# Optimization experiments

Hardware: AMD Instinct MI355X
Metric: run time of the kernel (lower is better)

## Reference

```python
import jax, jax.numpy as jnp
import numpy as np

H = 8        # num_heads
L = 2        # num_layers
F = 9        # num_fields
D = 128      # n_field_info
DH = D       # per-head depth = (D*H)//H
NB = 50      # n_base
EXCL = (0, 1, 2)  # fields excluded in FinalMerge (SelfAttention_Ex0, n_fields-3 inputs)
EPS = 1e-5


def _ln(x, g, b):
    m = jnp.mean(x, -1, keepdims=True)
    v = jnp.mean((x - m) ** 2, -1, keepdims=True)
    return (x - m) / jnp.sqrt(v + EPS) * g + b


def _forward(Y, Gin, posW1, posB1, posW2, posB2, posW3, posB3,
             Wq, bq, Wk, bk, Wv, bv, Wo, bo, lnG, lnB, fnG, fnB, poolW,
             uQW, uQB, uKW, uKB, uVW, uVB, mQW, mQB, mKW, mKB, mVW, mVB):
    B, S, _ = Y.shape
    pooled = []
    for f in range(F):  # per-field towers are structurally distinct (separate params)
        gy = jnp.concatenate([Y, Gin[:, :, f:f + 1]], axis=-1)        # [B,S,NB+1]
        h = jnp.tanh(gy @ posW1[f].T + posB1[f])
        h = jnp.tanh(h @ posW2[f].T + posB2[f])
        x = jax.nn.sigmoid(h @ posW3[f].T + posB3[f])                  # [B,S,D]
        for l in range(L):
            q = (x @ Wq[l, f].T + bq[l, f]).reshape(B, S, H, DH).transpose(0, 2, 1, 3)
            k = (x @ Wk[l, f].T + bk[l, f]).reshape(B, S, H, DH).transpose(0, 2, 1, 3)
            v = (x @ Wv[l, f].T + bv[l, f]).reshape(B, S, H, DH).transpose(0, 2, 1, 3)
            att = jax.nn.softmax(jnp.einsum('bhsd,bhtd->bhst', q, k) / jnp.sqrt(jnp.float32(DH)), axis=-1)
            wv = jnp.einsum('bhst,bhtd->bhsd', att, v).transpose(0, 2, 1, 3).reshape(B, S, H * DH)
            out = wv @ Wo[l, f].T + bo[l, f]
            x = _ln(x + out, lnG[l, f], lnB[l, f])   # residual + per-field LayerNorm
        x = _ln(x, fnG, fnB)                         # final_norm
        sc = jax.nn.softmax(x @ poolW[f][:, None], axis=1)             # GlobalAttentionPooling, [B,S,1]
        pooled.append(jnp.sum(x * sc, axis=1))                         # [B,D]
    U = jnp.stack(pooled, axis=-1)                                     # [B,D,F]

    unified = []
    for f in range(F):  # SelfAttention per target field
        Q = U @ uQW[f].T + uQB[f]                                      # [B,D,D]
        K = U @ uKW[f].T + uKB[f]
        V = U @ uVW[f].T + uVB[f]
        A = jax.nn.softmax(jnp.einsum('bik,bjk->bij', Q, K) / jnp.sqrt(jnp.float32(F)), axis=-1)
        o = jnp.einsum('bij,bjk->bik', A, V).mean(axis=-1)             # [B,D]
        o = o + (U[:, :, f] if f > 0 else U.mean(axis=-1))
        unified.append(o)
    Uu = jnp.stack(unified, axis=-1)                                   # [B,D,F]

    inc = [i for i in range(F) if i not in EXCL]
    Us = U[:, :, jnp.array(inc)]                                       # [B,D,F-3]
    Q = Us @ mQW.T + mQB
    K = Us @ mKW.T + mKB
    V = Us @ mVW.T + mVB
    A = jax.nn.softmax(jnp.einsum('bik,bjk->bij', Q, K) / jnp.sqrt(jnp.float32(F)), axis=-1)
    g = jnp.einsum('bij,bjk->bik', A, V).mean(axis=-1) + Us.mean(axis=-1)  # [B,D]
    return jnp.concatenate([Uu, g[:, :, None]], axis=-1)               # [B,D,F+1]


def setup_inputs() -> dict:
    key = jax.random.key(0)
    ks = iter(jax.random.split(key, 64))
    nrm = lambda shape, s=1.0: jax.random.normal(next(ks), shape, dtype=jnp.float32) * s
    B, S = 8, 512
    d = {}
    d['Y'] = nrm((B, S, NB))
    d['Gin'] = nrm((B, S, F))
    d['posW1'] = nrm((F, 50, NB + 1), 0.14); d['posB1'] = jnp.zeros((F, 50))
    d['posW2'] = nrm((F, 50, 50), 0.14);     d['posB2'] = jnp.zeros((F, 50))
    d['posW3'] = nrm((F, D, 50), 0.14);      d['posB3'] = jnp.zeros((F, D))
    d['Wq'] = nrm((L, F, H * DH, D), 0.09);  d['bq'] = jnp.zeros((L, F, H * DH))
    d['Wk'] = nrm((L, F, H * DH, D), 0.09);  d['bk'] = jnp.zeros((L, F, H * DH))
    d['Wv'] = nrm((L, F, H * DH, D), 0.09);  d['bv'] = jnp.zeros((L, F, H * DH))
    d['Wo'] = nrm((L, F, D, H * DH), 0.03);  d['bo'] = jnp.zeros((L, F, D))
    d['lnG'] = jnp.ones((L, F, D)); d['lnB'] = jnp.zeros((L, F, D))
    d['fnG'] = jnp.ones((D,));      d['fnB'] = jnp.zeros((D,))
    d['poolW'] = nrm((F, D))
    d['uQW'] = nrm((F, D, F), 0.33); d['uQB'] = jnp.zeros((F, D))
    d['uKW'] = nrm((F, D, F), 0.33); d['uKB'] = jnp.zeros((F, D))
    d['uVW'] = nrm((F, D, F), 0.33); d['uVB'] = jnp.zeros((F, D))
    d['mQW'] = nrm((D, F - 3), 0.4); d['mQB'] = jnp.zeros((D,))
    d['mKW'] = nrm((D, F - 3), 0.4); d['mKB'] = jnp.zeros((D,))
    d['mVW'] = nrm((D, F - 3), 0.4); d['mVB'] = jnp.zeros((D,))
    return d


def reference(Y, Gin, posW1, posB1, posW2, posB2, posW3, posB3,
              Wq, bq, Wk, bk, Wv, bv, Wo, bo, lnG, lnB, fnG, fnB, poolW,
              uQW, uQB, uKW, uKB, uVW, uVB, mQW, mQB, mKW, mKB, mVW, mVB):
    return _forward(Y, Gin, posW1, posB1, posW2, posB2, posW3, posB3,
                    Wq, bq, Wk, bk, Wv, bv, Wo, bo, lnG, lnB, fnG, fnB, poolW,
                    uQW, uQB, uKW, uKB, uVW, uVB, mQW, mQB, mKW, mKB, mVW, mVB)
```

## Files before the change

### kernel.cpp

```cpp
#include <hip/hip_runtime.h>
#include <hip/hip_bf16.h>

#define F_  9
#define B_  8
#define S_  512
#define H_  8
#define DH_ 128
#define D_  128
#define NB_ 50
#define BS_ 4096
#define PERBUF 4194304UL
#define WELEMS 2359296UL

typedef short bf16x8 __attribute__((ext_vector_type(8)));
typedef float f32x4  __attribute__((ext_vector_type(4)));
typedef unsigned int u32x4 __attribute__((ext_vector_type(4)));

static __device__ __forceinline__ unsigned short f2b(float f) {
    unsigned int u = __float_as_uint(f);
    unsigned int r = (u + 0x7FFFu + ((u >> 16) & 1u)) >> 16;
    return (unsigned short)r;
}
static __device__ __forceinline__ float b2f(unsigned short u) {
    return __uint_as_float(((unsigned int)u) << 16);
}
static __device__ __forceinline__ unsigned int cvtpk(float lo, float hi) {
    unsigned int r;
    asm("v_cvt_pk_bf16_f32 %0, %1, %2" : "=v"(r) : "v"(lo), "v"(hi));
    return r;
}

__global__ __launch_bounds__(256) void cvt4_kernel(
    const float* __restrict__ s0, const float* __restrict__ s1,
    const float* __restrict__ s2, const float* __restrict__ s3,
    unsigned short* __restrict__ d0, unsigned short* __restrict__ d1,
    unsigned short* __restrict__ d2, unsigned short* __restrict__ d3, int n)
{
    const float* s; unsigned short* d;
    switch (blockIdx.y) {
        case 0: s = s0; d = d0; break;
        case 1: s = s1; d = d1; break;
        case 2: s = s2; d = d2; break;
        default: s = s3; d = d3; break;
    }
    int i = (blockIdx.x * 256 + threadIdx.x) * 8;
    if (i + 8 <= n) {
        float4 a = *(const float4*)&s[i];
        float4 b = *(const float4*)&s[i + 4];
        ushort4 o0 = { f2b(a.x), f2b(a.y), f2b(a.z), f2b(a.w) };
        ushort4 o1 = { f2b(b.x), f2b(b.y), f2b(b.z), f2b(b.w) };
        *(ushort4*)&d[i]     = o0;
        *(ushort4*)&d[i + 4] = o1;
    }
}

__global__ __launch_bounds__(256) void posnet_kernel(
    const float* __restrict__ Y, const float* __restrict__ Gin,
    const float* __restrict__ W1g, const float* __restrict__ B1,
    const float* __restrict__ W2g, const float* __restrict__ B2,
    const float* __restrict__ W3g, const float* __restrict__ B3,
    float* __restrict__ xA, unsigned short* __restrict__ xAb)
{
    __shared__ float gys[4][8][52];
    __shared__ float hs[4][8][52];

    int f = blockIdx.y;
    int t = threadIdx.x, w = t >> 6, j = t & 63;
    int rowbase = blockIdx.x * 32 + w * 8;

#pragma unroll
    for (int rr = 0; rr < 8; ++rr) {
        int row = rowbase + rr;
        if (j < 50)       gys[w][rr][j]  = Y[(size_t)row*50 + j];
        else if (j == 50) gys[w][rr][50] = Gin[(size_t)row*F_ + f];
    }

    int jj = (j < 50) ? j : 0;

    {
        const float* wp = W1g + f*2550 + jj*51;
        float wreg[51];
#pragma unroll
        for (int kk = 0; kk < 51; ++kk) wreg[kk] = wp[kk];
        float bb = B1[f*50 + jj];
        float acc[8];
#pragma unroll
        for (int rr = 0; rr < 8; ++rr) acc[rr] = bb;
#pragma unroll
        for (int k4 = 0; k4 < 48; k4 += 4) {
#pragma unroll
            for (int rr = 0; rr < 8; ++rr) {
                float4 gv = *(const float4*)&gys[w][rr][k4];
                acc[rr] += wreg[k4]*gv.x + wreg[k4+1]*gv.y + wreg[k4+2]*gv.z + wreg[k4+3]*gv.w;
            }
        }
#pragma unroll
        for (int kk = 48; kk < 51; ++kk)
#pragma unroll
            for (int rr = 0; rr < 8; ++rr) acc[rr] += wreg[kk]*gys[w][rr][kk];
        if (j < 50) {
#pragma unroll
            for (int rr = 0; rr < 8; ++rr) hs[w][rr][j] = tanhf(acc[rr]);
        }
    }

    {
        const float* wp = W2g + f*2500 + jj*50;
        float wreg[50];
#pragma unroll
        for (int kk = 0; kk < 50; ++kk) wreg[kk] = wp[kk];
        float bb = B2[f*50 + jj];
        float acc[8];
#pragma unroll
        for (int rr = 0; rr < 8; ++rr) acc[rr] = bb;
#pragma unroll
        for (int k4 = 0; k4 < 48; k4 += 4) {
#pragma unroll
            for (int rr = 0; rr < 8; ++rr) {
                float4 gv = *(const float4*)&hs[w][rr][k4];
                acc[rr] += wreg[k4]*gv.x + wreg[k4+1]*gv.y + wreg[k4+2]*gv.z + wreg[k4+3]*gv.w;
            }
        }
#pragma unroll
        for (int kk = 48; kk < 50; ++kk)
#pragma unroll
            for (int rr = 0; rr < 8; ++rr) acc[rr] += wreg[kk]*hs[w][rr][kk];
        if (j < 50) {
#pragma unroll
            for (int rr = 0; rr < 8; ++rr) gys[w][rr][j] = tanhf(acc[rr]);
        }
    }

#pragma unroll 1
    for (int ppass = 0; ppass < 2; ++ppass) {
        const float* wp = W3g + f*6400 + (ppass*64 + j)*50;
        float wreg[50];
#pragma unroll
        for (int kk = 0; kk < 50; ++kk) wreg[kk] = wp[kk];
        float bb = B3[f*128 + ppass*64 + j];
        float acc[8];
#pragma unroll
        for (int rr = 0; rr < 8; ++rr) acc[rr] = bb;
#pragma unroll
        for (int k4 = 0; k4 < 48; k4 += 4) {
#pragma unroll
            for (int rr = 0; rr < 8; ++rr) {
                float4 gv = *(const float4*)&gys[w][rr][k4];
                acc[rr] += wreg[k4]*gv.x + wreg[k4+1]*gv.y + wreg[k4+2]*gv.z + wreg[k4+3]*gv.w;
            }
        }
#pragma unroll
        for (int kk = 48; kk < 50; ++kk)
#pragma unroll
            for (int rr = 0; rr < 8; ++rr) acc[rr] += wreg[kk]*gys[w][rr][kk];
#pragma unroll
        for (int rr = 0; rr < 8; ++rr) {
            float x = 1.f / (1.f + expf(-acc[rr]));
            size_t roff = ((size_t)f*BS_ + rowbase + rr)*128 + ppass*64 + j;
            xA[roff]  = x;
            xAb[roff] = f2b(x);
        }
    }
}

__global__ __launch_bounds__(256) void qkv_mfma_kernel(
    const unsigned short* __restrict__ xb,
    const unsigned short* __restrict__ Wqb, const unsigned short* __restrict__ Wkb,
    const unsigned short* __restrict__ Wvb,
    const float* __restrict__ bq, const float* __restrict__ bk, const float* __restrict__ bv,
    unsigned short* __restrict__ qo, unsigned short* __restrict__ ko,
    unsigned int* __restrict__ vto, int l, int f0)
{
    int z = blockIdx.z;
    int fl = z / 3, which = z - fl*3;
    int f = f0 + fl;
    const unsigned short* W; const float* bias;
    if (which == 0)      { W = Wqb; bias = bq; }
    else if (which == 1) { W = Wkb; bias = bk; }
    else                 { W = Wvb; bias = bv; }
    W    += (size_t)(l*F_ + f) * 1024 * 128;
    bias += (size_t)(l*F_ + f) * 1024;

    int m0 = blockIdx.x * 128;
    int n0 = blockIdx.y * 128;
    int t = threadIdx.x, w = t >> 6, ln = t & 63, g = ln >> 4, c = ln & 15;
    int wr = w >> 1, wc = w & 1;

    const unsigned short* Ab = xb + ((size_t)f*BS_ + m0 + wr*64)*128;
    const unsigned short* Bb = W + (size_t)(n0 + wc*64)*128;

    f32x4 acc[4][4];
#pragma unroll
    for (int mi = 0; mi < 4; ++mi)
#pragma unroll
        for (int ni = 0; ni < 4; ++ni) acc[mi][ni] = (f32x4){0.f,0.f,0.f,0.f};

#pragma unroll
    for (int kt = 0; kt < 4; ++kt) {
        bf16x8 af[4], bfr[4];
#pragma unroll
        for (int mi = 0; mi < 4; ++mi)
            af[mi] = *(const bf16x8*)&Ab[(size_t)(mi*16 + c)*128 + kt*32 + g*8];
#pragma unroll
        for (int ni = 0; ni < 4; ++ni)
            bfr[ni] = *(const bf16x8*)&Bb[(size_t)(ni*16 + c)*128 + kt*32 + g*8];
#pragma unroll
        for (int mi = 0; mi < 4; ++mi)
#pragma unroll
            for (int ni = 0; ni < 4; ++ni)
                acc[mi][ni] = __builtin_amdgcn_mfma_f32_16x16x32_bf16(af[mi], bfr[ni], acc[mi][ni], 0, 0, 0);
    }

    int h = n0 >> 7;
    float bs_[4];
#pragma unroll
    for (int ni = 0; ni < 4; ++ni) bs_[ni] = bias[n0 + wc*64 + ni*16 + c];

    if (which < 2) {
        float qscale = (which == 0) ? 0.08838834764831845f : 1.0f;
        unsigned short* out = (which == 0 ? qo : ko) + (size_t)fl * PERBUF;
#pragma unroll
        for (int mi = 0; mi < 4; ++mi) {
#pragma unroll
            for (int r = 0; r < 4; ++r) {
                int m = m0 + wr*64 + mi*16 + 4*g + r;
                int b = m >> 9, s = m & 511;
                unsigned short* orow = out + (((size_t)(b*H_ + h))*S_ + s)*128;
#pragma unroll
                for (int ni = 0; ni < 4; ++ni)
                    orow[wc*64 + ni*16 + c] = f2b((acc[mi][ni][r] + bs_[ni]) * qscale);
            }
        }
    } else {
        unsigned int* vtf = vto + (size_t)fl * (PERBUF/2);
#pragma unroll
        for (int mi = 0; mi < 4; ++mi) {
            int mbase = m0 + wr*64 + mi*16 + 4*g;
            int b = mbase >> 9, sh = (mbase & 511) >> 1;
            unsigned int* vtp = vtf + ((size_t)(b*H_ + h))*32768;
#pragma unroll
            for (int ni = 0; ni < 4; ++ni) {
                int d = wc*64 + ni*16 + c;
                float bb_ = bs_[ni];
                unsigned int p01 = (unsigned int)f2b(acc[mi][ni][0] + bb_)
                                 | ((unsigned int)f2b(acc[mi][ni][1] + bb_) << 16);
                unsigned int p23 = (unsigned int)f2b(acc[mi][ni][2] + bb_)
                                 | ((unsigned int)f2b(acc[mi][ni][3] + bb_) << 16);
                vtp[(size_t)d*256 + sh]     = p01;
                vtp[(size_t)d*256 + sh + 1] = p23;
            }
        }
    }
}

__global__ __launch_bounds__(256) void attn_mfma_kernel(
    const unsigned short* __restrict__ q, const unsigned short* __restrict__ k,
    const unsigned int* __restrict__ vt, unsigned short* __restrict__ wv)
{
    int t = threadIdx.x;
    int w = t >> 6, ln = t & 63, g = ln >> 4, c = ln & 15;
    int bid = blockIdx.x;
    int group = bid >> 5, within = bid & 31;
    int i = within >> 3, hl = within & 7;
    int hIdx = group*8 + hl;
    int fl = hIdx >> 6, by = hIdx & 63;
    int q0 = i*128 + w*32;

    const unsigned short* qh = q + ((size_t)(fl*64 + by))*S_*128;
    const unsigned short* kh = k + ((size_t)(fl*64 + by))*S_*128;
    const unsigned int*  vth = vt + ((size_t)(fl*64 + by))*32768;
    int b = by >> 3, h = by & 7;
    unsigned short* wvh = wv + ((size_t)(fl*B_ + b))*S_*1024 + h*128;

    __shared__ alignas(16) unsigned short Ks[2][32][136];
    __shared__ alignas(16) unsigned int   Vs[2][128][20];

    int krow = t >> 4, kseg = t & 15;
    int vrow = t >> 2, vseg = t & 3;

    bf16x8 qf[2][4];
#pragma unroll
    for (int gq = 0; gq < 2; ++gq)
#pragma unroll
        for (int d0 = 0; d0 < 4; ++d0)
            qf[gq][d0] = *(const bf16x8*)&qh[(size_t)(q0 + gq*16 + c)*128 + d0*32 + g*8];

    f32x4 acc[2][8];
#pragma unroll
    for (int gq = 0; gq < 2; ++gq)
#pragma unroll
        for (int i2 = 0; i2 < 8; ++i2) acc[gq][i2] = (f32x4){0.f, 0.f, 0.f, 0.f};
    float mrow[2] = {-1e30f, -1e30f};
    float lrow[2] = {0.f, 0.f};

    int srcA = ((g & 1) << 5) + c;
    int srcB = srcA + 16;
    bool glow = (g < 2);

    uint4 kr0, kr1, vr0, vr1;
    {
        kr0 = *(const uint4*)&kh[(size_t)krow*128 + kseg*8];
        kr1 = *(const uint4*)&kh[(size_t)(krow + 16)*128 + kseg*8];
        vr0 = *(const uint4*)&vth[(size_t)vrow*256 + vseg*4];
        vr1 = *(const uint4*)&vth[(size_t)(vrow + 64)*256 + vseg*4];
        *(uint4*)&Ks[0][krow][kseg*8]      = kr0;
        *(uint4*)&Ks[0][krow + 16][kseg*8] = kr1;
        *(uint4*)&Vs[0][vrow][vseg*4]      = vr0;
        *(uint4*)&Vs[0][vrow + 64][vseg*4] = vr1;
    }
    __syncthreads();

    int cur = 0;
    for (int kt = 0; kt < 16; ++kt) {
        if (kt < 15) {
            const unsigned short* ks = kh + (size_t)(kt + 1)*32*128;
            const unsigned int*  vsp = vth + (kt + 1)*16;
            kr0 = *(const uint4*)&ks[(size_t)krow*128 + kseg*8];
            kr1 = *(const uint4*)&ks[(size_t)(krow + 16)*128 + kseg*8];
            vr0 = *(const uint4*)&vsp[(size_t)vrow*256 + vseg*4];
            vr1 = *(const uint4*)&vsp[(size_t)(vrow + 64)*256 + vseg*4];
        }

        f32x4 s[2][2];
        s[0][0] = (f32x4){0.f,0.f,0.f,0.f}; s[0][1] = (f32x4){0.f,0.f,0.f,0.f};
        s[1][0] = (f32x4){0.f,0.f,0.f,0.f}; s[1][1] = (f32x4){0.f,0.f,0.f,0.f};
        __builtin_amdgcn_s_setprio(1);
#pragma unroll
        for (int d0 = 0; d0 < 4; ++d0) {
            bf16x8 k0 = *(const bf16x8*)&Ks[cur][c][g*8 + d0*32];
            bf16x8 k1 = *(const bf16x8*)&Ks[cur][16 + c][g*8 + d0*32];
#pragma unroll
            for (int gq = 0; gq < 2; ++gq) {
                s[gq][0] = __builtin_amdgcn_mfma_f32_16x16x32_bf16(k0, qf[gq][d0], s[gq][0], 0, 0, 0);
                s[gq][1] = __builtin_amdgcn_mfma_f32_16x16x32_bf16(k1, qf[gq][d0], s[gq][1], 0, 0, 0);
            }
        }
        __builtin_amdgcn_s_setprio(0);

        float corr[2];
        bf16x8 pa[2];
        bool need = false;
#pragma unroll
        for (int gq = 0; gq < 2; ++gq) {
            float t0 = fmaxf(fmaxf(fmaxf(s[gq][0][0], s[gq][0][1]), fmaxf(s[gq][0][2], s[gq][0][3])),
                             fmaxf(fmaxf(s[gq][1][0], s[gq][1][1]), fmaxf(s[gq][1][2], s[gq][1][3])));
            t0 = fmaxf(t0, __shfl_xor(t0, 16));
            t0 = fmaxf(t0, __shfl_xor(t0, 32));
            float mo = mrow[gq];
            float mn = (t0 > mo + 8.f) ? t0 : mo;
            float co = __expf(mo - mn);
            corr[gq] = co;
            mrow[gq] = mn;
            float p00 = __expf(s[gq][0][0] - mn), p01 = __expf(s[gq][0][1] - mn);
            float p02 = __expf(s[gq][0][2] - mn), p03 = __expf(s[gq][0][3] - mn);
            float p10 = __expf(s[gq][1][0] - mn), p11 = __expf(s[gq][1][1] - mn);
            float p12 = __expf(s[gq][1][2] - mn), p13 = __expf(s[gq][1][3] - mn);
            float ps = ((p00 + p01) + (p02 + p03)) + ((p10 + p11) + (p12 + p13));
            ps += __shfl_xor(ps, 16);
            ps += __shfl_xor(ps, 32);
            lrow[gq] = lrow[gq]*co + ps;
            need = need || (co != 1.0f);

            unsigned int pk0 = cvtpk(p00, p01), pk1 = cvtpk(p02, p03);
            unsigned int pk2 = cvtpk(p10, p11), pk3 = cvtpk(p12, p13);
            unsigned int a0 = __shfl(pk0, srcA), a1 = __shfl(pk1, srcA);
            unsigned int b0 = __shfl(pk0, srcB), b1 = __shfl(pk1, srcB);
            unsigned int c0 = __shfl(pk2, srcA), c1 = __shfl(pk3, srcA);
            unsigned int d0_ = __shfl(pk2, srcB), d1_ = __shfl(pk3, srcB);
            u32x4 pu;
            pu[0] = glow ? a0 : c0;
            pu[1] = glow ? a1 : c1;
            pu[2] = glow ? b0 : d0_;
            pu[3] = glow ? b1 : d1_;
            pa[gq] = __builtin_bit_cast(bf16x8, pu);
        }

        if (__any(need)) {
#pragma unroll
            for (int gq = 0; gq < 2; ++gq) {
                float cr0 = __shfl(corr[gq], 4*g + 0);
                float cr1 = __shfl(corr[gq], 4*g + 1);
                float cr2 = __shfl(corr[gq], 4*g + 2);
                float cr3 = __shfl(corr[gq], 4*g + 3);
#pragma unroll
                for (int i2 = 0; i2 < 8; ++i2) {
                    f32x4 a = acc[gq][i2];
                    a[0] *= cr0; a[1] *= cr1; a[2] *= cr2; a[3] *= cr3;
                    acc[gq][i2] = a;
                }
            }
        }

        __builtin_amdgcn_s_setprio(1);
#pragma unroll
        for (int i2 = 0; i2 < 8; ++i2) {
            bf16x8 vf = *(const bf16x8*)&Vs[cur][i2*16 + c][g*4];
            acc[0][i2] = __builtin_amdgcn_mfma_f32_16x16x32_bf16(pa[0], vf, acc[0][i2], 0, 0, 0);
            acc[1][i2] = __builtin_amdgcn_mfma_f32_16x16x32_bf16(pa[1], vf, acc[1][i2], 0, 0, 0);
        }
        __builtin_amdgcn_s_setprio(0);

        if (kt < 15) {
            __syncthreads();
            int nxt = cur ^ 1;
            *(uint4*)&Ks[nxt][krow][kseg*8]      = kr0;
            *(uint4*)&Ks[nxt][krow + 16][kseg*8] = kr1;
            *(uint4*)&Vs[nxt][vrow][vseg*4]      = vr0;
            *(uint4*)&Vs[nxt][vrow + 64][vseg*4] = vr1;
            __syncthreads();
            cur = nxt;
        }
    }

#pragma unroll
    for (int gq = 0; gq < 2; ++gq) {
        float invq = 1.0f / lrow[gq];
        float iv0 = __shfl(invq, 4*g + 0);
        float iv1 = __shfl(invq, 4*g + 1);
        float iv2 = __shfl(invq, 4*g + 2);
        float iv3 = __shfl(invq, 4*g + 3);
#pragma unroll
        for (int i2 = 0; i2 < 8; ++i2) {
            unsigned short* wp = &wvh[(size_t)(q0 + gq*16 + 4*g)*1024 + i2*16 + c];
            wp[0]    = f2b(acc[gq][i2][0]*iv0);
            wp[1024] = f2b(acc[gq][i2][1]*iv1);
            wp[2048] = f2b(acc[gq][i2][2]*iv2);
            wp[3072] = f2b(acc[gq][i2][3]*iv3);
        }
    }
}

__global__ __launch_bounds__(256) void outproj_ln_kernel(
    const unsigned short* __restrict__ wv, const unsigned short* __restrict__ Wob,
    const float* __restrict__ bo, float* __restrict__ xA,
    unsigned short* __restrict__ xAb,
    const float* __restrict__ lnGb, const float* __restrict__ lnBb,
    int l, int f0)
{
    __shared__ float Xs[128][132];

    int fl = blockIdx.z, f = f0 + fl;
    int m0 = blockIdx.x * 128;
    int t = threadIdx.x, w = t >> 6, ln = t & 63, g = ln >> 4, c = ln & 15;
    int wr = w >> 1, wc = w & 1;

    const unsigned short* Ab = wv + ((size_t)fl*BS_ + m0 + wr*64)*1024;
    const unsigned short* Bb = Wob + (size_t)(l*F_ + f)*128*1024 + (size_t)(wc*64)*1024;
    const float* bob = bo + (size_t)(l*F_ + f)*128;

    f32x4 acc[4][4];
#pragma unroll
    for (int mi = 0; mi < 4; ++mi)
#pragma unroll
        for (int ni = 0; ni < 4; ++ni) acc[mi][ni] = (f32x4){0.f,0.f,0.f,0.f};

#pragma unroll 4
    for (int kt = 0; kt < 32; ++kt) {
        bf16x8 af[4], bfr[4];
#pragma unroll
        for (int mi = 0; mi < 4; ++mi)
            af[mi] = *(const bf16x8*)&Ab[(size_t)(mi*16 + c)*1024 + kt*32 + g*8];
#pragma unroll
        for (int ni = 0; ni < 4; ++ni)
            bfr[ni] = *(const bf16x8*)&Bb[(size_t)(ni*16 + c)*1024 + kt*32 + g*8];
#pragma unroll
        for (int mi = 0; mi < 4; ++mi)
#pragma unroll
            for (int ni = 0; ni < 4; ++ni)
                acc[mi][ni] = __builtin_amdgcn_mfma_f32_16x16x32_bf16(af[mi], bfr[ni], acc[mi][ni], 0, 0, 0);
    }

    float bs_[4];
#pragma unroll
    for (int ni = 0; ni < 4; ++ni) bs_[ni] = bob[wc*64 + ni*16 + c];

#pragma unroll
    for (int mi = 0; mi < 4; ++mi) {
#pragma unroll
        for (int r = 0; r < 4; ++r) {
            int lm = wr*64 + mi*16 + 4*g + r;
            const float* xr = xA + ((size_t)f*BS_ + m0 + lm)*128;
#pragma unroll
            for (int ni = 0; ni < 4; ++ni) {
                int n = wc*64 + ni*16 + c;
                Xs[lm][n] = acc[mi][ni][r] + bs_[ni] + xr[n];
            }
        }
    }
    __syncthreads();

    const float* gp = lnGb + (size_t)fl*128;
    const float* bp = lnBb + (size_t)fl*128;
    float g0 = gp[ln], g1 = gp[64 + ln];
    float b0 = bp[ln], b1 = bp[64 + ln];
#pragma unroll 1
    for (int rr = w; rr < 128; rr += 4) {
        float a = Xs[rr][ln], cv = Xs[rr][64 + ln];
        float s = a + cv;
#pragma unroll
        for (int off = 1; off < 64; off <<= 1) s += __shfl_xor(s, off);
        float mean = s * (1.0f/128.0f);
        float da = a - mean, dc = cv - mean;
        float vs = da*da + dc*dc;
#pragma unroll
        for (int off = 1; off < 64; off <<= 1) vs += __shfl_xor(vs, off);
        float inv = rsqrtf(vs * (1.0f/128.0f) + 1e-5f);
        float o0 = da*inv*g0 + b0;
        float o1 = dc*inv*g1 + b1;
        size_t row = (size_t)f*BS_ + m0 + rr;
        xA[row*128 + ln]       = o0;
        xA[row*128 + 64 + ln]  = o1;
        xAb[row*128 + ln]      = f2b(o0);
        xAb[row*128 + 64 + ln] = f2b(o1);
    }
}

__global__ __launch_bounds__(256) void ln_kernel(
    const float* __restrict__ xin, float* __restrict__ xout,
    unsigned short* __restrict__ xoutb,
    const float* __restrict__ g, const float* __restrict__ bb, int f0, int gstride)
{
    int t = threadIdx.x, lane = t & 63, w = t >> 6;
    int rowl = blockIdx.x * 4 + w;
    int fl = rowl >> 12;
    size_t row = (size_t)f0*BS_ + rowl;
    const float* xi = xin + row*128;
    float a = xi[lane], c = xi[64 + lane];
    float s = a + c;
#pragma unroll
    for (int off = 1; off < 64; off <<= 1) s += __shfl_xor(s, off);
    float mean = s * (1.0f/128.0f);
    float da = a - mean, dc = c - mean;
    float vs = da*da + dc*dc;
#pragma unroll
    for (int off = 1; off < 64; off <<= 1) vs += __shfl_xor(vs, off);
    float inv = rsqrtf(vs * (1.0f/128.0f) + 1e-5f);
    const float* gp = g + (size_t)fl*gstride;
    const float* bp = bb + (size_t)fl*gstride;
    float o0 = da*inv*gp[lane]      + bp[lane];
    float o1 = dc*inv*gp[64 + lane] + bp[64 + lane];
    float* xo = xout + row*128;
    xo[lane]      = o0;
    xo[64 + lane] = o1;
    xoutb[row*128 + lane]      = f2b(o0);
    xoutb[row*128 + 64 + lane] = f2b(o1);
}

__global__ __launch_bounds__(256) void pool_kernel(
    const float* __restrict__ xB, const float* __restrict__ poolW,
    float* __restrict__ U, int f0)
{
    int f = f0 + blockIdx.x, b = blockIdx.y;
    const float* xb = xB + ((size_t)f*BS_ + (size_t)b*S_)*128;
    const float* pw = poolW + f*128;
    __shared__ float sc[512];
    __shared__ float red[8];
    __shared__ float MS[2];
    __shared__ float pool2[256];
    int t = threadIdx.x, lane = t & 63, w = t >> 6;

    float p0 = pw[lane], p1 = pw[64 + lane];
    for (int s = w; s < 512; s += 4) {
        float a = xb[(size_t)s*128 + lane]*p0 + xb[(size_t)s*128 + 64 + lane]*p1;
#pragma unroll
        for (int off = 1; off < 64; off <<= 1) a += __shfl_xor(a, off);
        if (lane == 0) sc[s] = a;
    }
    __syncthreads();

    float m = -1e30f;
    for (int s = t; s < 512; s += 256) m = fmaxf(m, sc[s]);
#pragma unroll
    for (int off = 1; off < 64; off <<= 1) m = fmaxf(m, __shfl_xor(m, off));
    if (lane == 0) red[w] = m;
    __syncthreads();
    if (t == 0) MS[0] = fmaxf(fmaxf(red[0], red[1]), fmaxf(red[2], red[3]));
    __syncthreads();
    float M = MS[0];

    float ssum = 0.f;
    for (int s = t; s < 512; s += 256) { float e = expf(sc[s] - M); sc[s] = e; ssum += e; }
#pragma unroll
    for (int off = 1; off < 64; off <<= 1) ssum += __shfl_xor(ssum, off);
    if (lane == 0) red[4 + w] = ssum;
    __syncthreads();
    if (t == 0) MS[1] = red[4] + red[5] + red[6] + red[7];
    __syncthreads();
    float inv = 1.0f / MS[1];

    int d = t & 127, hh = t >> 7;
    float a = 0.f;
    for (int s = hh*256; s < hh*256 + 256; ++s) a += sc[s]*xb[(size_t)s*128 + d];
    pool2[t] = a;
    __syncthreads();
    if (t < 128) U[((size_t)b*128 + d)*F_ + f] = (pool2[t] + pool2[t + 128]) * inv;
}

__global__ __launch_bounds__(256) void unified_kernel(
    const float* __restrict__ U,
    const float* __restrict__ uQW, const float* __restrict__ uQB,
    const float* __restrict__ uKW, const float* __restrict__ uKB,
    const float* __restrict__ uVW, const float* __restrict__ uVB,
    float* __restrict__ outp)
{
    int f = blockIdx.x, b = blockIdx.y;
    __shared__ float Ub[128*9];
    __shared__ float Wj[128*9];
    __shared__ float zj[128];
    __shared__ float vm[128];
    __shared__ float Mm[81];
    __shared__ float wvm[9], bvec[9];
    __shared__ float cc_[2];
    int t = threadIdx.x;
    for (int i = t; i < 1152; i += 256) Ub[i] = U[(size_t)b*1152 + i];
    const float* qw = uQW + (size_t)f*1152;
    const float* kw = uKW + (size_t)f*1152;
    const float* vw = uVW + (size_t)f*1152;
    const float* qb = uQB + (size_t)f*128;
    const float* kb = uKB + (size_t)f*128;
    const float* vb = uVB + (size_t)f*128;

    if (t < 81) {
        int t1 = t/9, s1 = t%9; float a = 0.f;
        for (int kk = 0; kk < 128; ++kk) a += qw[kk*9 + t1]*kw[kk*9 + s1];
        Mm[t] = a;
    } else if (t < 90) {
        int s1 = t - 81; float a = 0.f;
        for (int kk = 0; kk < 128; ++kk) a += kw[kk*9 + s1]*qb[kk];
        bvec[s1] = a;
    } else if (t < 99) {
        int t1 = t - 90; float a = 0.f;
        for (int kk = 0; kk < 128; ++kk) a += vw[kk*9 + t1];
        wvm[t1] = a * (1.0f/128.0f);
    } else if (t == 99) {
        float a = 0.f, c2 = 0.f;
        for (int kk = 0; kk < 128; ++kk) { a += qb[kk]*kb[kk]; c2 += vb[kk]; }
        cc_[0] = a; cc_[1] = c2 * (1.0f/128.0f);
    }
    __syncthreads();

    if (t < 128) {
        int j = t;
        for (int t1 = 0; t1 < 9; ++t1) {
            float a = 0.f;
            for (int s1 = 0; s1 < 9; ++s1) a += Mm[t1*9 + s1]*Ub[j*9 + s1];
            Wj[j*9 + t1] = a;
        }
        float z = cc_[0], v2 = cc_[1];
        for (int s1 = 0; s1 < 9; ++s1) { z += bvec[s1]*Ub[j*9 + s1]; v2 += wvm[s1]*Ub[j*9 + s1]; }
        zj[j] = z; vm[j] = v2;
    }
    __syncthreads();

    int i = t >> 1, half = t & 1;
    float ui[9];
#pragma unroll
    for (int s1 = 0; s1 < 9; ++s1) ui[s1] = Ub[i*9 + s1];

    float mx = -1e30f;
    for (int jj = 0; jj < 64; ++jj) {
        int j = half*64 + jj;
        float a = zj[j];
#pragma unroll
        for (int s1 = 0; s1 < 9; ++s1) a += ui[s1]*Wj[j*9 + s1];
        mx = fmaxf(mx, a * (1.0f/3.0f));
    }
    mx = fmaxf(mx, __shfl_xor(mx, 1));
    float sum = 0.f, o = 0.f;
    for (int jj = 0; jj < 64; ++jj) {
        int j = half*64 + jj;
        float a = zj[j];
#pragma unroll
        for (int s1 = 0; s1 < 9; ++s1) a += ui[s1]*Wj[j*9 + s1];
        float p = expf(a * (1.0f/3.0f) - mx);
        sum += p; o += p*vm[j];
    }
    sum += __shfl_xor(sum, 1);
    o   += __shfl_xor(o, 1);
    if (half == 0) {
        float base;
        if (f > 0) base = ui[f];
        else { base = 0.f; for (int s1 = 0; s1 < 9; ++s1) base += ui[s1]; base *= (1.0f/9.0f); }
        outp[((size_t)b*128 + i)*10 + f] = o/sum + base;
    }
}

__global__ __launch_bounds__(256) void merge_kernel(
    const float* __restrict__ U,
    const float* __restrict__ mQW, const float* __restrict__ mQB,
    const float* __restrict__ mKW, const float* __restrict__ mKB,
    const float* __restrict__ mVW, const float* __restrict__ mVB,
    float* __restrict__ outp)
{
    int b = blockIdx.x;
    __shared__ float Us[128*6];
    __shared__ float Wj[128*6];
    __shared__ float zj[128];
    __shared__ float vm[128];
    __shared__ float Mm[36];
    __shared__ float wvm[6], bvec[6];
    __shared__ float cc_[2];
    int t = threadIdx.x;
    for (int i = t; i < 768; i += 256) {
        int j = i/6, tt = i - j*6;
        Us[i] = U[(size_t)b*1152 + j*9 + 3 + tt];
    }
    if (t < 36) {
        int t1 = t/6, s1 = t%6; float a = 0.f;
        for (int kk = 0; kk < 128; ++kk) a += mQW[kk*6 + t1]*mKW[kk*6 + s1];
        Mm[t] = a;
    } else if (t < 42) {
        int s1 = t - 36; float a = 0.f;
        for (int kk = 0; kk < 128; ++kk) a += mKW[kk*6 + s1]*mQB[kk];
        bvec[s1] = a;
    } else if (t < 48) {
        int t1 = t - 42; float a = 0.f;
        for (int kk = 0; kk < 128; ++kk) a += mVW[kk*6 + t1];
        wvm[t1] = a * (1.0f/128.0f);
    } else if (t == 48) {
        float a = 0.f, c2 = 0.f;
        for (int kk = 0; kk < 128; ++kk) { a += mQB[kk]*mKB[kk]; c2 += mVB[kk]; }
        cc_[0] = a; cc_[1] = c2 * (1.0f/128.0f);
    }
    __syncthreads();

    if (t < 128) {
        int j = t;
        for (int t1 = 0; t1 < 6; ++t1) {
            float a = 0.f;
            for (int s1 = 0; s1 < 6; ++s1) a += Mm[t1*6 + s1]*Us[j*6 + s1];
            Wj[j*6 + t1] = a;
        }
        float z = cc_[0], v2 = cc_[1];
        for (int s1 = 0; s1 < 6; ++s1) { z += bvec[s1]*Us[j*6 + s1]; v2 += wvm[s1]*Us[j*6 + s1]; }
        zj[j] = z; vm[j] = v2;
    }
    __syncthreads();

    int i = t >> 1, half = t & 1;
    float ui[6];
#pragma unroll
    for (int s1 = 0; s1 < 6; ++s1) ui[s1] = Us[i*6 + s1];

    float mx = -1e30f;
    for (int jj = 0; jj < 64; ++jj) {
        int j = half*64 + jj;
        float a = zj[j];
#pragma unroll
        for (int s1 = 0; s1 < 6; ++s1) a += ui[s1]*Wj[j*6 + s1];
        mx = fmaxf(mx, a * (1.0f/3.0f));
    }
    mx = fmaxf(mx, __shfl_xor(mx, 1));
    float sum = 0.f, o = 0.f;
    for (int jj = 0; jj < 64; ++jj) {
        int j = half*64 + jj;
        float a = zj[j];
#pragma unroll
        for (int s1 = 0; s1 < 6; ++s1) a += ui[s1]*Wj[j*6 + s1];
        float p = expf(a * (1.0f/3.0f) - mx);
        sum += p; o += p*vm[j];
    }
    sum += __shfl_xor(sum, 1);
    o   += __shfl_xor(o, 1);
    if (half == 0) {
        float base = 0.f;
        for (int s1 = 0; s1 < 6; ++s1) base += ui[s1];
        base *= (1.0f/6.0f);
        outp[((size_t)b*128 + i)*10 + 9] = o/sum + base;
    }
}

extern "C" void kernel_launch(void* const* d_in, const int* in_sizes, int n_in,
                              void* d_out, int out_size, void* d_ws, size_t ws_size,
                              hipStream_t stream)
{
    const float* Y     = (const float*)d_in[0];
    const float* Gin   = (const float*)d_in[1];
    const float* posW1 = (const float*)d_in[2];
    const float* posB1 = (const float*)d_in[3];
    const float* posW2 = (const float*)d_in[4];
    const float* posB2 = (const float*)d_in[5];
    const float* posW3 = (const float*)d_in[6];
    const float* posB3 = (const float*)d_in[7];
    const float* Wq    = (const float*)d_in[8];
    const float* bq    = (const float*)d_in[9];
    const float* Wk    = (const float*)d_in[10];
    const float* bk    = (const float*)d_in[11];
    const float* Wv    = (const float*)d_in[12];
    const float* bv    = (const float*)d_in[13];
    const float* Wo    = (const float*)d_in[14];
    const float* bo    = (const float*)d_in[15];
    const float* lnG   = (const float*)d_in[16];
    const float* lnB   = (const float*)d_in[17];
    const float* fnG   = (const float*)d_in[18];
    const float* fnB   = (const float*)d_in[19];
    const float* poolW = (const float*)d_in[20];
    const float* uQW   = (const float*)d_in[21];
    const float* uQB   = (const float*)d_in[22];
    const float* uKW   = (const float*)d_in[23];
    const float* uKB   = (const float*)d_in[24];
    const float* uVW   = (const float*)d_in[25];
    const float* uVB   = (const float*)d_in[26];
    const float* mQW   = (const float*)d_in[27];
    const float* mQB   = (const float*)d_in[28];
    const float* mKW   = (const float*)d_in[29];
    const float* mKB   = (const float*)d_in[30];
    const float* mVW   = (const float*)d_in[31];
    const float* mVB   = (const float*)d_in[32];

    const size_t xelems = (size_t)F_ * BS_ * 128;
    char* p = (char*)d_ws;
    float* xA   = (float*)p;               p += xelems*4;
    float* xB   = (float*)p;               p += xelems*4;
    float* Ubuf = (float*)p;               p += 16384*4;
    unsigned short* xAb = (unsigned short*)p; p += xelems*2;
    unsigned short* Wqb = (unsigned short*)p; p += WELEMS*2;
    unsigned short* Wkb = (unsigned short*)p; p += WELEMS*2;
    unsigned short* Wvb = (unsigned short*)p; p += WELEMS*2;
    unsigned short* Wob = (unsigned short*)p; p += WELEMS*2;
    size_t fixed_bytes = (size_t)(p - (char*)d_ws);

    size_t avail = (ws_size > fixed_bytes) ? (ws_size - fixed_bytes) : 0;
    size_t per_f = 8UL * PERBUF;
    int FC = (int)(avail / per_f);
    if (FC < 1) FC = 1;
    if (FC > F_) FC = F_;

    unsigned short* qb  = (unsigned short*)p;
    unsigned short* kb  = qb + (size_t)FC*PERBUF;
    unsigned short* wvb = kb + (size_t)FC*PERBUF;
    unsigned int*   vtb = (unsigned int*)(wvb + (size_t)FC*PERBUF);

    {
        int n = (int)WELEMS, gx = (n/8 + 255)/256;
        cvt4_kernel<<<dim3(gx, 4), 256, 0, stream>>>(
            Wq, Wk, Wv, Wo, Wqb, Wkb, Wvb, Wob, n);
    }

    posnet_kernel<<<dim3(128, F_), 256, 0, stream>>>(
        Y, Gin, posW1, posB1, posW2, posB2, posW3, posB3, xA, xAb);

    for (int l = 0; l < 2; ++l) {
        for (int f0 = 0; f0 < F_; f0 += FC) {
            int fc = (F_ - f0) < FC ? (F_ - f0) : FC;
            qkv_mfma_kernel<<<dim3(32, 8, 3*fc), 256, 0, stream>>>(
                xAb, Wqb, Wkb, Wvb, bq, bk, bv, qb, kb, vtb, l, f0);
            attn_mfma_kernel<<<dim3(256*fc), 256, 0, stream>>>(qb, kb, vtb, wvb);
            outproj_ln_kernel<<<dim3(32, 1, fc), 256, 0, stream>>>(
                wvb, Wob, bo, xA, xAb,
                lnG + (size_t)(l*F_ + f0)*128, lnB + (size_t)(l*F_ + f0)*128, l, f0);
        }
    }

    for (int f0 = 0; f0 < F_; f0 += FC) {
        int fc = (F_ - f0) < FC ? (F_ - f0) : FC;
        ln_kernel<<<dim3(fc*1024), 256, 0, stream>>>(xA, xB, xAb, fnG, fnB, f0, 0);
        pool_kernel<<<dim3(fc, 8), 256, 0, stream>>>(xB, poolW, Ubuf, f0);
    }

    unified_kernel<<<dim3(F_, B_), 256, 0, stream>>>(
        Ubuf, uQW, uQB, uKW, uKB, uVW, uVB, (float*)d_out);
    merge_kernel<<<dim3(B_), 256, 0, stream>>>(
        Ubuf, mQW, mQB, mKW, mKB, mVW, mVB, (float*)d_out);
}
```

Baseline: 1.087 ms.

## Repad attention LDS tiles, drop a barrier, and retile out-projection to 64-row blocks

The attention kernel shrinks LDS row padding for K and V tiles, switching to 8-byte LDS accesses so the new strides stay aligned and bank-friendly. It also removes the barrier before writing the next double buffer. The out-projection+LayerNorm kernel now uses 64-row blocks with each wave owning 16 rows across all 128 columns, doubling the grid and cutting per-thread accumulators to raise occupancy. Removing the pre-write barrier risks a race: a fast wave can overwrite buffer nxt while slower waves still read it from the previous iteration, and 8-byte accesses double LDS instruction count.

Measured after the change: 1.201 ms. +10.5%, slower.

```diff
diff --git a/kernel.cpp b/kernel.cpp
--- a/kernel.cpp
+++ b/kernel.cpp
@@ -29,6 +29,18 @@
     asm("v_cvt_pk_bf16_f32 %0, %1, %2" : "=v"(r) : "v"(lo), "v"(hi));
     return r;
 }
+static __device__ __forceinline__ bf16x8 ld8s(const unsigned short* p) {
+    uint2 lo = *(const uint2*)p;
+    uint2 hi = *(const uint2*)(p + 4);
+    u32x4 u; u[0] = lo.x; u[1] = lo.y; u[2] = hi.x; u[3] = hi.y;
+    return __builtin_bit_cast(bf16x8, u);
+}
+static __device__ __forceinline__ bf16x8 ld8v(const unsigned int* p) {
+    uint2 lo = *(const uint2*)p;
+    uint2 hi = *(const uint2*)(p + 2);
+    u32x4 u; u[0] = lo.x; u[1] = lo.y; u[2] = hi.x; u[3] = hi.y;
+    return __builtin_bit_cast(bf16x8, u);
+}
 
 __global__ __launch_bounds__(256) void cvt4_kernel(
     const float* __restrict__ s0, const float* __restrict__ s1,
@@ -272,8 +284,8 @@
     int b = by >> 3, h = by & 7;
     unsigned short* wvh = wv + ((size_t)(fl*B_ + b))*S_*1024 + h*128;
 
-    __shared__ alignas(16) unsigned short Ks[2][32][136];
-    __shared__ alignas(16) unsigned int   Vs[2][128][20];
+    __shared__ alignas(16) unsigned short Ks[2][32][132];
+    __shared__ alignas(16) unsigned int   Vs[2][128][18];
 
     int krow = t >> 4, kseg = t & 15;
     int vrow = t >> 2, vseg = t & 3;
@@ -303,10 +315,14 @@
         kr1 = *(const uint4*)&kh[(size_t)(krow + 16)*128 + kseg*8];
         vr0 = *(const uint4*)&vth[(size_t)vrow*256 + vseg*4];
         vr1 = *(const uint4*)&vth[(size_t)(vrow + 64)*256 + vseg*4];
-        *(uint4*)&Ks[0][krow][kseg*8]      = kr0;
-        *(uint4*)&Ks[0][krow + 16][kseg*8] = kr1;
-        *(uint4*)&Vs[0][vrow][vseg*4]      = vr0;
-        *(uint4*)&Vs[0][vrow + 64][vseg*4] = vr1;
+        *(uint2*)&Ks[0][krow][kseg*8]          = make_uint2(kr0.x, kr0.y);
+        *(uint2*)&Ks[0][krow][kseg*8 + 4]      = make_uint2(kr0.z, kr0.w);
+        *(uint2*)&Ks[0][krow + 16][kseg*8]     = make_uint2(kr1.x, kr1.y);
+        *(uint2*)&Ks[0][krow + 16][kseg*8 + 4] = make_uint2(kr1.z, kr1.w);
+        *(uint2*)&Vs[0][vrow][vseg*4]          = make_uint2(vr0.x, vr0.y);
+        *(uint2*)&Vs[0][vrow][vseg*4 + 2]      = make_uint2(vr0.z, vr0.w);
+        *(uint2*)&Vs[0][vrow + 64][vseg*4]     = make_uint2(vr1.x, vr1.y);
+        *(uint2*)&Vs[0][vrow + 64][vseg*4 + 2] = make_uint2(vr1.z, vr1.w);
     }
     __syncthreads();
 
@@ -327,8 +343,8 @@
         __builtin_amdgcn_s_setprio(1);
 #pragma unroll
         for (int d0 = 0; d0 < 4; ++d0) {
-            bf16x8 k0 = *(const bf16x8*)&Ks[cur][c][g*8 + d0*32];
-            bf16x8 k1 = *(const bf16x8*)&Ks[cur][16 + c][g*8 + d0*32];
+            bf16x8 k0 = ld8s(&Ks[cur][c][g*8 + d0*32]);
+            bf16x8 k1 = ld8s(&Ks[cur][16 + c][g*8 + d0*32]);
 #pragma unroll
             for (int gq = 0; gq < 2; ++gq) {
                 s[gq][0] = __builtin_amdgcn_mfma_f32_16x16x32_bf16(k0, qf[gq][d0], s[gq][0], 0, 0, 0);
@@ -394,19 +410,22 @@
         __builtin_amdgcn_s_setprio(1);
 #pragma unroll
         for (int i2 = 0; i2 < 8; ++i2) {
-            bf16x8 vf = *(const bf16x8*)&Vs[cur][i2*16 + c][g*4];
+            bf16x8 vf = ld8v(&Vs[cur][i2*16 + c][g*4]);
             acc[0][i2] = __builtin_amdgcn_mfma_f32_16x16x32_bf16(pa[0], vf, acc[0][i2], 0, 0, 0);
             acc[1][i2] = __builtin_amdgcn_mfma_f32_16x16x32_bf16(pa[1], vf, acc[1][i2], 0, 0, 0);
         }
         __builtin_amdgcn_s_setprio(0);
 
         if (kt < 15) {
-            __syncthreads();
             int nxt = cur ^ 1;
-            *(uint4*)&Ks[nxt][krow][kseg*8]      = kr0;
-            *(uint4*)&Ks[nxt][krow + 16][kseg*8] = kr1;
-            *(uint4*)&Vs[nxt][vrow][vseg*4]      = vr0;
-            *(uint4*)&Vs[nxt][vrow + 64][vseg*4] = vr1;
+            *(uint2*)&Ks[nxt][krow][kseg*8]          = make_uint2(kr0.x, kr0.y);
+            *(uint2*)&Ks[nxt][krow][kseg*8 + 4]      = make_uint2(kr0.z, kr0.w);
+            *(uint2*)&Ks[nxt][krow + 16][kseg*8]     = make_uint2(kr1.x, kr1.y);
+            *(uint2*)&Ks[nxt][krow + 16][kseg*8 + 4] = make_uint2(kr1.z, kr1.w);
+            *(uint2*)&Vs[nxt][vrow][vseg*4]          = make_uint2(vr0.x, vr0.y);
+            *(uint2*)&Vs[nxt][vrow][vseg*4 + 2]      = make_uint2(vr0.z, vr0.w);
+            *(uint2*)&Vs[nxt][vrow + 64][vseg*4]     = make_uint2(vr1.x, vr1.y);
+            *(uint2*)&Vs[nxt][vrow + 64][vseg*4 + 2] = make_uint2(vr1.z, vr1.w);
             __syncthreads();
             cur = nxt;
         }
@@ -437,54 +456,38 @@
     const float* __restrict__ lnGb, const float* __restrict__ lnBb,
     int l, int f0)
 {
-    __shared__ float Xs[128][132];
+    __shared__ float Xs[64][132];
 
     int fl = blockIdx.z, f = f0 + fl;
-    int m0 = blockIdx.x * 128;
+    int m0 = blockIdx.x * 64;
     int t = threadIdx.x, w = t >> 6, ln = t & 63, g = ln >> 4, c = ln & 15;
-    int wr = w >> 1, wc = w & 1;
-
-    const unsigned short* Ab = wv + ((size_t)fl*BS_ + m0 + wr*64)*1024;
-    const unsigned short* Bb = Wob + (size_t)(l*F_ + f)*128*1024 + (size_t)(wc*64)*1024;
+
+    const unsigned short* Ab = wv + ((size_t)fl*BS_ + m0 + w*16)*1024;
+    const unsigned short* Bb = Wob + (size_t)(l*F_ + f)*128*1024;
     const float* bob = bo + (size_t)(l*F_ + f)*128;
 
-    f32x4 acc[4][4];
-#pragma unroll
-    for (int mi = 0; mi < 4; ++mi)
-#pragma unroll
-        for (int ni = 0; ni < 4; ++ni) acc[mi][ni] = (f32x4){0.f,0.f,0.f,0.f};
+    f32x4 acc[8];
+#pragma unroll
+    for (int ni = 0; ni < 8; ++ni) acc[ni] = (f32x4){0.f,0.f,0.f,0.f};
 
 #pragma unroll 4
     for (int kt = 0; kt < 32; ++kt) {
-        bf16x8 af[4], bfr[4];
-#pragma unroll
-        for (int mi = 0; mi < 4; ++mi)
-            af[mi] = *(const bf16x8*)&Ab[(size_t)(mi*16 + c)*1024 + kt*32 + g*8];
-#pragma unroll
-        for (int ni = 0; ni < 4; ++ni)
-            bfr[ni] = *(const bf16x8*)&Bb[(size_t)(ni*16 + c)*1024 + kt*32 + g*8];
-#pragma unroll
-        for (int mi = 0; mi < 4; ++mi)
-#pragma unroll
-            for (int ni = 0; ni < 4; ++ni)
-                acc[mi][ni] = __builtin_amdgcn_mfma_f32_16x16x32_bf16(af[mi], bfr[ni], acc[mi][ni], 0, 0, 0);
-    }
-
-    float bs_[4];
-#pragma unroll
-    for (int ni = 0; ni < 4; ++ni) bs_[ni] = bob[wc*64 + ni*16 + c];
-
-#pragma unroll
-    for (int mi = 0; mi < 4; ++mi) {
-#pragma unroll
-        for (int r = 0; r < 4; ++r) {
-            int lm = wr*64 + mi*16 + 4*g + r;
-            const float* xr = xA + ((size_t)f*BS_ + m0 + lm)*128;
-#pragma unroll
-            for (int ni = 0; ni < 4; ++ni) {
-                int n = wc*64 + ni*16 + c;
-                Xs[lm][n] = acc[mi][ni][r] + bs_[ni] + xr[n];
-            }
+        bf16x8 af = *(const bf16x8*)&Ab[(size_t)c*1024 + kt*32 + g*8];
+#pragma unroll
+        for (int ni = 0; ni < 8; ++ni) {
+            bf16x8 bfr = *(const bf16x8*)&Bb[(size_t)(ni*16 + c)*1024 + kt*32 + g*8];
+            acc[ni] = __builtin_amdgcn_mfma_f32_16x16x32_bf16(af, bfr, acc[ni], 0, 0, 0);
+        }
+    }
+
+#pragma unroll
+    for (int r = 0; r < 4; ++r) {
+        int lm = w*16 + 4*g + r;
+        const float* xr = xA + ((size_t)f*BS_ + m0 + lm)*128;
+#pragma unroll
+        for (int ni = 0; ni < 8; ++ni) {
+            int n = ni*16 + c;
+            Xs[lm][n] = acc[ni][r] + bob[n] + xr[n];
         }
     }
     __syncthreads();
@@ -494,7 +497,7 @@
     float g0 = gp[ln], g1 = gp[64 + ln];
     float b0 = bp[ln], b1 = bp[64 + ln];
 #pragma unroll 1
-    for (int rr = w; rr < 128; rr += 4) {
+    for (int rr = w; rr < 64; rr += 4) {
         float a = Xs[rr][ln], cv = Xs[rr][64 + ln];
         float s = a + cv;
 #pragma unroll
@@ -846,7 +849,7 @@
             qkv_mfma_kernel<<<dim3(32, 8, 3*fc), 256, 0, stream>>>(
                 xAb, Wqb, Wkb, Wvb, bq, bk, bv, qb, kb, vtb, l, f0);
             attn_mfma_kernel<<<dim3(256*fc), 256, 0, stream>>>(qb, kb, vtb, wvb);
-            outproj_ln_kernel<<<dim3(32, 1, fc), 256, 0, stream>>>(
+            outproj_ln_kernel<<<dim3(64, 1, fc), 256, 0, stream>>>(
                 wvb, Wob, bo, xA, xAb,
                 lnG + (size_t)(l*F_ + f0)*128, lnB + (size_t)(l*F_ + f0)*128, l, f0);
         }
```
